# Kernel tuning notes

Hardware: AMD Instinct MI355X
Metric: run time of the kernel (lower is better)

Reference implementation:

```python
import jax, jax.numpy as jnp
import numpy as np
import math

L = 4          # n_layers
H = 8          # n_heads
TOP_K = 32
Z99 = 2.326347874040841
SQRT2PI = math.sqrt(2.0 * math.pi)
CONF = 0.99
SCALE_MAX = 1.0  # model not calibrated -> _scale_max = 1.0
EPS = 1e-5


def layer_norm(x, g, b):
    m = jnp.mean(x, axis=-1, keepdims=True)
    v = jnp.var(x, axis=-1, keepdims=True)
    return (x - m) * jax.lax.rsqrt(v + EPS) * g + b


def pos_encoding(T, D):
    pos = jnp.arange(T, dtype=jnp.float32)[:, None]
    div = jnp.exp(jnp.arange(0, D, 2, dtype=jnp.float32) * (-math.log(10000.0) / D))
    pe = jnp.zeros((T, D), jnp.float32)
    pe = pe.at[:, 0::2].set(jnp.sin(pos * div))
    pe = pe.at[:, 1::2].set(jnp.cos(pos * div))
    return pe  # [T, D]


def sparse_attn(h, Wq, Wk, Wv, Wo, bo):
    B, T, D = h.shape
    dh = D // H
    q = (h @ Wq).reshape(B, T, H, dh)
    k = (h @ Wk).reshape(B, T, H, dh)
    v = (h @ Wv).reshape(B, T, H, dh)
    scores = jnp.einsum('bthd,bshd->bhts', q, k) / np.float32(np.sqrt(dh))  # [B,H,T,T]
    kth = jax.lax.top_k(scores, TOP_K)[0][..., -1:]  # k-th largest per row
    scores = jnp.where(scores < kth, -jnp.inf, scores)
    attn = jax.nn.softmax(scores, axis=-1)
    attn = jnp.nan_to_num(attn)
    out = jnp.einsum('bhts,bshd->bthd', attn, v).reshape(B, T, D)
    return out @ Wo + bo


def encoder_layer(h, Wq, Wk, Wv, Wo, bo, W1, b1, W2, b2, g1, be1, g2, be2):
    h = layer_norm(h + sparse_attn(h, Wq, Wk, Wv, Wo, bo), g1, be1)
    ff = jax.nn.gelu((h @ W1) + b1, approximate=False) @ W2 + b2
    return layer_norm(h + ff, g2, be2)


def setup_inputs() -> dict:
    key = jax.random.key(0)
    B, T, Din, D, Dff = 16, 1024, 64, 512, 2048
    ks = jax.random.split(key, 12)

    def p(k, shape):
        return jax.random.normal(k, shape, jnp.float32) * np.float32(1.0 / np.sqrt(shape[-2]))

    return {
        'x': jax.random.normal(ks[0], (B, T, Din), jnp.float32),
        'W_in': p(ks[1], (Din, D)), 'b_in': jnp.zeros((D,), jnp.float32),
        'Wq': p(ks[2], (L, D, D)), 'Wk': p(ks[3], (L, D, D)),
        'Wv': p(ks[4], (L, D, D)), 'Wo': p(ks[5], (L, D, D)),
        'bo': jnp.zeros((L, D), jnp.float32),
        'W1': p(ks[6], (L, D, Dff)), 'b1': jnp.zeros((L, Dff), jnp.float32),
        'W2': p(ks[7], (L, Dff, D)), 'b2': jnp.zeros((L, D), jnp.float32),
        'g1': jnp.ones((L, D), jnp.float32), 'be1': jnp.zeros((L, D), jnp.float32),
        'g2': jnp.ones((L, D), jnp.float32), 'be2': jnp.zeros((L, D), jnp.float32),
        'gm': jnp.ones((D,), jnp.float32), 'bm': jnp.zeros((D,), jnp.float32),
        'Wm': p(ks[8], (D, 1)), 'cm': jnp.zeros((1,), jnp.float32),
        'gs': jnp.ones((D,), jnp.float32), 'bs': jnp.zeros((D,), jnp.float32),
        'Ws': p(ks[9], (D, 1)), 'cs': jnp.zeros((1,), jnp.float32),
    }


def reference(x, W_in, b_in, Wq, Wk, Wv, Wo, bo, W1, b1, W2, b2, g1, be1, g2, be2,
              gm, bm, Wm, cm, gs, bs, Ws, cs):
    B, T, _ = x.shape
    D = W_in.shape[1]
    h = (x @ W_in) + b_in + pos_encoding(T, D)[None]  # input_proj + pos enc (dropout=eval)
    for i in range(L):
        h = encoder_layer(h, Wq[i], Wk[i], Wv[i], Wo[i], bo[i],
                          W1[i], b1[i], W2[i], b2[i], g1[i], be1[i], g2[i], be2[i])
    h_last = h[:, -1, :]  # [B, D]
    mu = (layer_norm(h_last, gm, bm) @ Wm + cm)[:, 0]
    scale = jax.nn.sigmoid(layer_norm(h_last, gs, bs) @ Ws + cs)[:, 0] * SCALE_MAX
    var_pred = mu + scale * Z99
    phi_z = math.exp(-0.5 * Z99 ** 2) / SQRT2PI
    es_pred = mu + scale * phi_z / (1.0 - CONF)
    return jnp.stack([mu, scale, var_pred, es_pred])  # [4, B]
```

## Files before the change

### kernel.cpp

```cpp
#include <hip/hip_runtime.h>
#include <math.h>


typedef unsigned int u32;
typedef __attribute__((ext_vector_type(8))) _Float16 f16x8;
typedef __attribute__((ext_vector_type(4))) float f32x4;

__device__ __forceinline__ void g2l16(const void* g, void* l) {
  __builtin_amdgcn_global_load_lds(
      (const __attribute__((address_space(1))) u32*)g,
      (__attribute__((address_space(3))) u32*)l, 16, 0, 0);
}

__device__ __forceinline__ void wsplit(float w, unsigned short* ph, unsigned short* pl) {
  _Float16 hi = (_Float16)w;
  _Float16 lo = (_Float16)(w - (float)hi);
  union { _Float16 h; unsigned short u; } a, b; a.h = hi; b.h = lo;
  *ph = a.u; *pl = b.u;
}

__global__ __launch_bounds__(256) void wprep_kernel(const float* __restrict__ src,
    unsigned short* __restrict__ dst_hi, unsigned short* __restrict__ dst_lo,
    int K, int N) {
  __shared__ float t[64][65];
  const int k0 = blockIdx.y * 64, n0 = blockIdx.x * 64;
#pragma unroll
  for (int i = 0; i < 16; i++) {
    int idx = threadIdx.x + i * 256;
    int kk = idx >> 6, nn = idx & 63;
    t[kk][nn] = src[(size_t)(k0 + kk) * N + n0 + nn];
  }
  __syncthreads();
#pragma unroll
  for (int i = 0; i < 16; i++) {
    int idx = threadIdx.x + i * 256;
    int nn = idx >> 6, kk = idx & 63;
    unsigned short uh, ul;
    wsplit(t[kk][nn], &uh, &ul);
    dst_hi[(size_t)(n0 + nn) * K + k0 + kk] = uh;
    dst_lo[(size_t)(n0 + nn) * K + k0 + kk] = ul;
  }
}

__global__ __launch_bounds__(256) void wprep4_kernel(
    const float* __restrict__ s0, const float* __restrict__ s1,
    const float* __restrict__ s2, const float* __restrict__ s3,
    unsigned short* __restrict__ h0, unsigned short* __restrict__ h1,
    unsigned short* __restrict__ h2, unsigned short* __restrict__ h3,
    unsigned short* __restrict__ l0, unsigned short* __restrict__ l1,
    unsigned short* __restrict__ l2, unsigned short* __restrict__ l3) {
  __shared__ float t[64][65];
  const float* src = blockIdx.z == 0 ? s0 : blockIdx.z == 1 ? s1 : blockIdx.z == 2 ? s2 : s3;
  unsigned short* dh = blockIdx.z == 0 ? h0 : blockIdx.z == 1 ? h1 : blockIdx.z == 2 ? h2 : h3;
  unsigned short* dl = blockIdx.z == 0 ? l0 : blockIdx.z == 1 ? l1 : blockIdx.z == 2 ? l2 : l3;
  const int k0 = blockIdx.y * 64, n0 = blockIdx.x * 64;
#pragma unroll
  for (int i = 0; i < 16; i++) {
    int idx = threadIdx.x + i * 256;
    int kk = idx >> 6, nn = idx & 63;
    t[kk][nn] = src[(size_t)(k0 + kk) * 512 + n0 + nn];
  }
  __syncthreads();
#pragma unroll
  for (int i = 0; i < 16; i++) {
    int idx = threadIdx.x + i * 256;
    int nn = idx >> 6, kk = idx & 63;
    unsigned short uh, ul;
    wsplit(t[kk][nn], &uh, &ul);
    dh[(size_t)(n0 + nn) * 512 + k0 + kk] = uh;
    dl[(size_t)(n0 + nn) * 512 + k0 + kk] = ul;
  }
}

__global__ __launch_bounds__(256) void gemm_split(const float* __restrict__ A,
    const unsigned short* __restrict__ Bhi, const unsigned short* __restrict__ Blo,
    const float* __restrict__ bias, float* __restrict__ C,
    unsigned short* __restrict__ Ph, unsigned short* __restrict__ Pl,
    int M, int N, int K, int ldb, int epi) {
  __shared__ float          As[128 * 64];
  __shared__ unsigned short BsH[128 * 64];
  __shared__ unsigned short BsL[128 * 64];
  const int tid = threadIdx.x;
  const int w = tid >> 6, l = tid & 63;
  const int wm = w >> 1, wn = w & 1;
  const int bm = blockIdx.y * 128, bn = blockIdx.x * 128;
  f32x4 acc[4][4] = {};

  for (int k0 = 0; k0 < K; k0 += 64) {
    if (k0) __syncthreads();
#pragma unroll
    for (int i = 0; i < 8; i++) {
      int cl = i * 256 + w * 64 + l;
      int row = cl >> 4, c = cl & 15;
      int col = (((c >> 1) ^ (row & 7)) * 8) + (c & 1) * 4;
      g2l16(A + (size_t)(bm + row) * K + k0 + col, As + (size_t)(i * 256 + w * 64) * 4);
    }
#pragma unroll
    for (int i = 0; i < 4; i++) {
      int cl = i * 256 + w * 64 + l;
      int row = cl >> 3, c = cl & 7;
      int col = ((c ^ (row & 7)) * 8);
      size_t src = (size_t)(bn + row) * ldb + k0 + col;
      g2l16(Bhi + src, BsH + (size_t)(i * 256 + w * 64) * 8);
      g2l16(Blo + src, BsL + (size_t)(i * 256 + w * 64) * 8);
    }
    __syncthreads();
#pragma unroll
    for (int kk = 0; kk < 2; kk++) {
      f16x8 ahi[4], alo[4], bhi[4], blo[4];
      const int c16 = kk * 4 + (l >> 4);
#pragma unroll
      for (int i = 0; i < 4; i++) {
        int ar = wm * 64 + i * 16 + (l & 15);
        const float* ap = &As[ar * 64 + ((c16 ^ (ar & 7)) * 8)];
        float4 a0 = *(const float4*)ap;
        float4 a1 = *(const float4*)(ap + 4);
        float av[8] = {a0.x, a0.y, a0.z, a0.w, a1.x, a1.y, a1.z, a1.w};
#pragma unroll
        for (int e = 0; e < 8; e++) {
          _Float16 hh = (_Float16)av[e];
          ahi[i][e] = hh;
          alo[i][e] = (_Float16)(av[e] - (float)hh);
        }
        int br = wn * 64 + i * 16 + (l & 15);
        bhi[i] = *(const f16x8*)&BsH[br * 64 + ((c16 ^ (br & 7)) * 8)];
        blo[i] = *(const f16x8*)&BsL[br * 64 + ((c16 ^ (br & 7)) * 8)];
      }
#pragma unroll
      for (int i = 0; i < 4; i++)
#pragma unroll
        for (int j = 0; j < 4; j++) {
          acc[i][j] = __builtin_amdgcn_mfma_f32_16x16x32_f16(ahi[i], bhi[j], acc[i][j], 0, 0, 0);
          acc[i][j] = __builtin_amdgcn_mfma_f32_16x16x32_f16(alo[i], bhi[j], acc[i][j], 0, 0, 0);
          acc[i][j] = __builtin_amdgcn_mfma_f32_16x16x32_f16(ahi[i], blo[j], acc[i][j], 0, 0, 0);
        }
    }
  }

  if (epi == 5) {
#pragma unroll
    for (int i = 0; i < 4; i++)
#pragma unroll
      for (int e = 0; e < 4; e++) {
        int row = bm + wm * 64 + i * 16 + (l >> 4) * 4 + e;
#pragma unroll
        for (int j = 0; j < 4; j++) {
          int col = bn + wn * 64 + j * 16 + (l & 15);
          float vv = acc[i][j][e];
          unsigned short uh, ul;
          wsplit(vv, &uh, &ul);
          size_t off = (size_t)(row >> 10) * 524288 + (size_t)(col >> 6) * 65536
                     + (size_t)(row & 1023) * 64 + (col & 63);
          Ph[off] = uh; Pl[off] = ul;
        }
      }
    return;
  }

  float bj[4], fr[4];
#pragma unroll
  for (int j = 0; j < 4; j++) {
    int col = bn + wn * 64 + j * 16 + (l & 15);
    bj[j] = (bias != nullptr) ? bias[col] : 0.f;
    fr[j] = (epi == 3) ? __expf((float)(col & ~1) * (-9.210340371976184f / 512.0f)) : 0.f;
  }
#pragma unroll
  for (int i = 0; i < 4; i++) {
#pragma unroll
    for (int e = 0; e < 4; e++) {
      int row = bm + wm * 64 + i * 16 + (l >> 4) * 4 + e;
#pragma unroll
      for (int j = 0; j < 4; j++) {
        int col = bn + wn * 64 + j * 16 + (l & 15);
        float v = acc[i][j][e] + bj[j];
        if (epi == 2) v = 0.5f * v * (1.0f + erff(v * 0.70710678118654752f));
        if (epi == 3) {
          float ang = (float)(row & 1023) * fr[j];
          v += (col & 1) ? cosf(ang) : sinf(ang);
        }
        if (epi == 4) v += C[(size_t)row * N + col];
        C[(size_t)row * N + col] = v;
      }
    }
  }
}

__device__ __forceinline__ unsigned f2o(float f) {
  unsigned b = __float_as_uint(f);
  return (b & 0x80000000u) ? ~b : (b | 0x80000000u);
}
__device__ __forceinline__ float o2f(unsigned u) {
  unsigned b = (u & 0x80000000u) ? (u & 0x7fffffffu) : ~u;
  return __uint_as_float(b);
}

__global__ __launch_bounds__(512, 4) void attn_kernel(
    const unsigned short* __restrict__ qh, const unsigned short* __restrict__ ql,
    const unsigned short* __restrict__ kh, const unsigned short* __restrict__ kl,
    const float* __restrict__ va, float* __restrict__ ao) {
  __shared__ __align__(16) float smem[14464];
  unsigned short* Qhs = (unsigned short*)smem;
  unsigned short* Qls = Qhs + 2048;
  unsigned short* Khs = Qhs + 4096;
  unsigned short* Kls = Qhs + 12288;
  float* S    = smem + 10240;
  float* cval = smem + 2048;
  int*   cidx = (int*)smem + 5376;

  const int tid = threadIdx.x;
  const int wave = tid >> 6, lane = tid & 63;
  const int id = blockIdx.x;
  const int bh = (id >> 8) * 8 + (id & 7);
  const int t0 = ((id >> 3) & 31) * 32;
  const int b = bh >> 3, hh = bh & 7;
  const size_t hoff = (size_t)bh * 65536;
  const float* vb = va + (size_t)b * 524288 + hh * 64;

  {
    int plane = tid >> 8, cl = tid & 255;
    int row = cl >> 3, c = cl & 7;
    size_t src = hoff + (size_t)(t0 + row) * 64 + ((c ^ (row & 7)) * 8);
    g2l16((plane ? ql : qh) + src, (plane ? Qls : Qhs) + cl * 8);
  }

  float sc[4][16];

  for (int kt = 0; kt < 8; ++kt) {
#pragma unroll
    for (int i = 0; i < 2; ++i) {
      int cl = tid + i * 512;
      int row = cl >> 3, c = cl & 7;
      size_t src = hoff + (size_t)(kt * 128 + row) * 64 + ((c ^ (row & 7)) * 8);
      g2l16(kh + src, Khs + cl * 8);
      g2l16(kl + src, Kls + cl * 8);
    }
    __syncthreads();

    f32x4 a0 = {}, a1 = {};
#pragma unroll
    for (int ks = 0; ks < 2; ++ks) {
      int c = (lane >> 4) + ks * 4;
      int kr = wave * 16 + (lane & 15);
      int ko = kr * 64 + ((c ^ (kr & 7)) * 8);
      f16x8 kfh = *(const f16x8*)&Khs[ko];
      f16x8 kfl = *(const f16x8*)&Kls[ko];
      int q0 = lane & 15;
      int o0 = q0 * 64 + ((c ^ (q0 & 7)) * 8);
      f16x8 qf0h = *(const f16x8*)&Qhs[o0];
      f16x8 qf0l = *(const f16x8*)&Qls[o0];
      int q1 = 16 + (lane & 15);
      int o1 = q1 * 64 + ((c ^ (q1 & 7)) * 8);
      f16x8 qf1h = *(const f16x8*)&Qhs[o1];
      f16x8 qf1l = *(const f16x8*)&Qls[o1];
      a0 = __builtin_amdgcn_mfma_f32_16x16x32_f16(kfh, qf0h, a0, 0, 0, 0);
      a0 = __builtin_amdgcn_mfma_f32_16x16x32_f16(kfl, qf0h, a0, 0, 0, 0);
      a0 = __builtin_amdgcn_mfma_f32_16x16x32_f16(kfh, qf0l, a0, 0, 0, 0);
      a1 = __builtin_amdgcn_mfma_f32_16x16x32_f16(kfh, qf1h, a1, 0, 0, 0);
      a1 = __builtin_amdgcn_mfma_f32_16x16x32_f16(kfl, qf1h, a1, 0, 0, 0);
      a1 = __builtin_amdgcn_mfma_f32_16x16x32_f16(kfh, qf1l, a1, 0, 0, 0);
    }
#pragma unroll
    for (int e = 0; e < 4; ++e) {
      int srow = wave * 16 + (lane >> 4) * 4 + e;
      S[srow * 33 + (lane & 15)]      = a0[e];
      S[srow * 33 + 16 + (lane & 15)] = a1[e];
    }
    __syncthreads();
#pragma unroll
    for (int r = 0; r < 4; ++r) {
      int qr = wave * 4 + r;
      sc[r][kt * 2]     = S[lane * 33 + qr] * 0.125f;
      sc[r][kt * 2 + 1] = S[(64 + lane) * 33 + qr] * 0.125f;
    }
    __syncthreads();
  }

  unsigned uu[4][16];
#pragma unroll
  for (int r = 0; r < 4; ++r)
#pragma unroll
    for (int j = 0; j < 16; ++j) uu[r][j] = f2o(sc[r][j]);

#pragma unroll
  for (int r = 0; r < 4; ++r) {
    const int row = wave * 4 + r;
    unsigned m = uu[r][0];
#pragma unroll
    for (int j = 1; j < 16; ++j) m = m > uu[r][j] ? m : uu[r][j];
    unsigned gm = m;
#pragma unroll
    for (int off = 32; off; off >>= 1) {
      unsigned o = __shfl_xor(gm, off);
      gm = gm > o ? gm : o;
    }
    unsigned lam = 0;
    for (int bit = 31; bit >= 16; --bit) {
      unsigned tv = lam | (1u << bit);
      if (__popcll(__ballot(m >= tv)) >= 32) lam = tv;
    }
    int base = 0;
#pragma unroll
    for (int j = 0; j < 16; ++j) {
      bool p = uu[r][j] >= lam;
      unsigned long long mk = __ballot(p);
      int pos = base + (int)__popcll(mk & ((1ull << lane) - 1ull));
      if (p && pos < 96) { cval[row * 104 + pos] = o2f(uu[r][j]); cidx[row * 104 + pos] = j * 64 + lane; }
      base += (int)__popcll(mk);
    }
    int C = base;
    unsigned kth = 0;
    if (C <= 96) {
      unsigned cu0 = (lane < C)      ? f2o(cval[row * 104 + lane])      : 0u;
      unsigned cu1 = (64 + lane < C) ? f2o(cval[row * 104 + 64 + lane]) : 0u;
      for (int bit = 31; bit >= 0; --bit) {
        unsigned tv = kth | (1u << bit);
        int c = (int)__popcll(__ballot(cu0 >= tv)) + (int)__popcll(__ballot(cu1 >= tv));
        if (c >= 32) kth = tv;
      }
    } else {
      for (int bit = 31; bit >= 0; --bit) {
        unsigned tv = kth | (1u << bit);
        int pc = 0;
#pragma unroll
        for (int j = 0; j < 16; ++j) pc += (uu[r][j] >= tv) ? 1 : 0;
#pragma unroll
        for (int off = 32; off; off >>= 1) pc += __shfl_xor(pc, off);
        if (pc >= 32) kth = tv;
      }
      base = 0;
#pragma unroll
      for (int j = 0; j < 16; ++j) {
        bool p = uu[r][j] >= kth;
        unsigned long long mk = __ballot(p);
        int pos = base + (int)__popcll(mk & ((1ull << lane) - 1ull));
        if (p && pos < 96) { cval[row * 104 + pos] = o2f(uu[r][j]); cidx[row * 104 + pos] = j * 64 + lane; }
        base += (int)__popcll(mk);
      }
      C = base < 96 ? base : 96;
    }
    float kth_f = o2f(kth), gm_f = o2f(gm);
    float e0 = 0.f, e1 = 0.f;
    if (lane < C)      { float vv = cval[row * 104 + lane];      if (vv >= kth_f) e0 = __expf(vv - gm_f); }
    if (64 + lane < C) { float vv = cval[row * 104 + 64 + lane]; if (vv >= kth_f) e1 = __expf(vv - gm_f); }
    float ps = e0 + e1;
#pragma unroll
    for (int off = 32; off; off >>= 1) ps += __shfl_xor(ps, off);
    cval[row * 104 + lane] = e0;
    if (lane < 32) cval[row * 104 + 64 + lane] = e1;
    if (lane < 8)  cval[row * 104 + 96 + lane] = 0.f;
    { int p = C + lane;      if (p < 104) cidx[row * 104 + p] = 0; }
    { int p = C + 64 + lane; if (p < 104) cidx[row * 104 + p] = 0; }

    float acc = 0.f;
    int C8 = (C + 7) & ~7;
    for (int i0 = 0; i0 < C8; i0 += 8) {
      float4 ev0 = *(const float4*)&cval[row * 104 + i0];
      float4 ev1 = *(const float4*)&cval[row * 104 + i0 + 4];
      int4  si0 = *(const int4*)&cidx[row * 104 + i0];
      int4  si1 = *(const int4*)&cidx[row * 104 + i0 + 4];
      float v0 = vb[(size_t)(si0.x & 1023) * 512 + lane];
      float v1 = vb[(size_t)(si0.y & 1023) * 512 + lane];
      float v2 = vb[(size_t)(si0.z & 1023) * 512 + lane];
      float v3 = vb[(size_t)(si0.w & 1023) * 512 + lane];
      float v4 = vb[(size_t)(si1.x & 1023) * 512 + lane];
      float v5 = vb[(size_t)(si1.y & 1023) * 512 + lane];
      float v6 = vb[(size_t)(si1.z & 1023) * 512 + lane];
      float v7 = vb[(size_t)(si1.w & 1023) * 512 + lane];
      acc = fmaf(ev0.x, v0, acc); acc = fmaf(ev0.y, v1, acc);
      acc = fmaf(ev0.z, v2, acc); acc = fmaf(ev0.w, v3, acc);
      acc = fmaf(ev1.x, v4, acc); acc = fmaf(ev1.y, v5, acc);
      acc = fmaf(ev1.z, v6, acc); acc = fmaf(ev1.w, v7, acc);
    }
    ao[((size_t)(b * 1024 + t0 + row)) * 512 + hh * 64 + lane] = acc * (1.f / ps);
  }
}

__global__ __launch_bounds__(256) void resid_ln_kernel(float* __restrict__ h,
    const float* __restrict__ o, const float* __restrict__ g,
    const float* __restrict__ be) {
  const int wave = threadIdx.x >> 6, lane = threadIdx.x & 63;
  const size_t row = (size_t)blockIdx.x * 4 + wave;
  float* hr = h + row * 512;
  const float* orr = o + row * 512;
  float x[8]; float s = 0.f, s2 = 0.f;
#pragma unroll
  for (int j = 0; j < 8; j++) {
    float vv = hr[j * 64 + lane] + orr[j * 64 + lane];
    x[j] = vv; s += vv; s2 += vv * vv;
  }
#pragma unroll
  for (int off = 32; off; off >>= 1) { s += __shfl_xor(s, off); s2 += __shfl_xor(s2, off); }
  float mean = s * (1.f / 512.f);
  float var  = s2 * (1.f / 512.f) - mean * mean;
  float r = rsqrtf(var + 1e-5f);
#pragma unroll
  for (int j = 0; j < 8; j++) {
    int d = j * 64 + lane;
    hr[d] = (x[j] - mean) * r * g[d] + be[d];
  }
}

__global__ __launch_bounds__(256) void head_kernel(const float* __restrict__ h,
    const float* __restrict__ gm, const float* __restrict__ bm,
    const float* __restrict__ Wm, const float* __restrict__ cm,
    const float* __restrict__ gs, const float* __restrict__ bs,
    const float* __restrict__ Ws, const float* __restrict__ cs,
    float* __restrict__ out) {
  const int wave = threadIdx.x >> 6, lane = threadIdx.x & 63;
  const int b = blockIdx.x * 4 + wave;
  const float* hr = h + ((size_t)b * 1024 + 1023) * 512;
  float x[8]; float s = 0.f, s2 = 0.f;
#pragma unroll
  for (int j = 0; j < 8; j++) { float vv = hr[j * 64 + lane]; x[j] = vv; s += vv; s2 += vv * vv; }
#pragma unroll
  for (int off = 32; off; off >>= 1) { s += __shfl_xor(s, off); s2 += __shfl_xor(s2, off); }
  float mean = s * (1.f / 512.f);
  float var  = s2 * (1.f / 512.f) - mean * mean;
  float r = rsqrtf(var + 1e-5f);
  float am = 0.f, as = 0.f;
#pragma unroll
  for (int j = 0; j < 8; j++) {
    int d = j * 64 + lane;
    float n = (x[j] - mean) * r;
    am = fmaf(n * gm[d] + bm[d], Wm[d], am);
    as = fmaf(n * gs[d] + bs[d], Ws[d], as);
  }
#pragma unroll
  for (int off = 32; off; off >>= 1) { am += __shfl_xor(am, off); as += __shfl_xor(as, off); }
  if (lane == 0) {
    const double Z = 2.326347874040841;
    float mu  = am + cm[0];
    float scl = 1.f / (1.f + expf(-(as + cs[0])));
    float esc = (float)(exp(-0.5 * Z * Z) / sqrt(2.0 * 3.14159265358979323846) / 0.01);
    out[b]      = mu;
    out[16 + b] = scl;
    out[32 + b] = mu + scl * (float)Z;
    out[48 + b] = mu + scl * esc;
  }
}

extern "C" void kernel_launch(void* const* d_in, const int* in_sizes, int n_in,
                              void* d_out, int out_size, void* d_ws, size_t ws_size,
                              hipStream_t stream) {
  const float* x    = (const float*)d_in[0];
  const float* W_in = (const float*)d_in[1];
  const float* b_in = (const float*)d_in[2];
  const float* Wq   = (const float*)d_in[3];
  const float* Wk   = (const float*)d_in[4];
  const float* Wv   = (const float*)d_in[5];
  const float* Wo   = (const float*)d_in[6];
  const float* bo   = (const float*)d_in[7];
  const float* W1   = (const float*)d_in[8];
  const float* b1   = (const float*)d_in[9];
  const float* W2   = (const float*)d_in[10];
  const float* b2   = (const float*)d_in[11];
  const float* g1   = (const float*)d_in[12];
  const float* be1  = (const float*)d_in[13];
  const float* g2   = (const float*)d_in[14];
  const float* be2  = (const float*)d_in[15];
  const float* gm   = (const float*)d_in[16];
  const float* bm   = (const float*)d_in[17];
  const float* Wm   = (const float*)d_in[18];
  const float* cm   = (const float*)d_in[19];
  const float* gs   = (const float*)d_in[20];
  const float* bs   = (const float*)d_in[21];
  const float* Ws   = (const float*)d_in[22];
  const float* cs   = (const float*)d_in[23];

  const int M = 16384, D = 512, DFF = 2048;
  float* ws = (float*)d_ws;
  float* h   = ws;
  unsigned short* qhp = (unsigned short*)(ws + 8388608);
  unsigned short* qlp = qhp + 8388608;
  unsigned short* khp = (unsigned short*)(ws + 16777216);
  unsigned short* klp = khp + 8388608;
  float* v   = ws + 25165824;
  float* ao  = ws + 33554432;
  float* ff  = ws + 8388608;
  unsigned short* wl = (unsigned short*)(ws + 41943040);
  unsigned short* WqH = wl,            *WqL = wl + 262144;
  unsigned short* WkH = wl + 524288,   *WkL = wl + 786432;
  unsigned short* WvH = wl + 1048576,  *WvL = wl + 1310720;
  unsigned short* WoH = wl + 1572864,  *WoL = wl + 1835008;
  unsigned short* W1H = wl + 2097152,  *W1L = wl + 3145728;
  unsigned short* W2H = wl + 4194304,  *W2L = wl + 5242880;
  unsigned short* WinH = (unsigned short*)(ws + 45088768);
  unsigned short* WinL = WinH + 32768;

  dim3 blk(256);
  dim3 gD(4, 128);
  dim3 gH(8, 128);

  wprep_kernel<<<dim3(8, 1, 1), blk, 0, stream>>>(W_in, WinH, WinL, 64, 512);
  gemm_split<<<gD, blk, 0, stream>>>(x, WinH, WinL, b_in, h, nullptr, nullptr, M, D, 64, 64, 3);

  for (int l = 0; l < 4; l++) {
    const float* wq = Wq + (size_t)l * 262144;
    const float* wk = Wk + (size_t)l * 262144;
    const float* wv = Wv + (size_t)l * 262144;
    const float* wo = Wo + (size_t)l * 262144;
    const float* w1 = W1 + (size_t)l * 1048576;
    const float* w2 = W2 + (size_t)l * 1048576;

    wprep4_kernel<<<dim3(8, 8, 4), blk, 0, stream>>>(wq, wk, wv, wo,
        WqH, WkH, WvH, WoH, WqL, WkL, WvL, WoL);
    wprep_kernel<<<dim3(32, 8, 1), blk, 0, stream>>>(w1, W1H, W1L, 512, 2048);
    wprep_kernel<<<dim3(8, 32, 1), blk, 0, stream>>>(w2, W2H, W2L, 2048, 512);

    gemm_split<<<gD, blk, 0, stream>>>(h, WqH, WqL, nullptr, nullptr, qhp, qlp, M, D, D, D, 5);
    gemm_split<<<gD, blk, 0, stream>>>(h, WkH, WkL, nullptr, nullptr, khp, klp, M, D, D, D, 5);
    gemm_split<<<gD, blk, 0, stream>>>(h, WvH, WvL, nullptr, v, nullptr, nullptr, M, D, D, D, 1);

    attn_kernel<<<dim3(4096), dim3(512), 0, stream>>>(qhp, qlp, khp, klp, v, ao);

    gemm_split<<<gD, blk, 0, stream>>>(ao, WoH, WoL, bo + (size_t)l * D, v, nullptr, nullptr, M, D, D, D, 1);
    resid_ln_kernel<<<dim3(4096), blk, 0, stream>>>(h, v, g1 + (size_t)l * D, be1 + (size_t)l * D);

    gemm_split<<<gH, blk, 0, stream>>>(h, W1H, W1L, b1 + (size_t)l * DFF, ff, nullptr, nullptr, M, 1024, D, D, 2);
    gemm_split<<<gD, blk, 0, stream>>>(ff, W2H, W2L, nullptr, ao, nullptr, nullptr, M, D, 1024, DFF, 1);
    gemm_split<<<gH, blk, 0, stream>>>(h, W1H + 524288, W1L + 524288,
                                       b1 + (size_t)l * DFF + 1024, ff, nullptr, nullptr, M, 1024, D, D, 2);
    gemm_split<<<gD, blk, 0, stream>>>(ff, W2H + 1024, W2L + 1024,
                                       b2 + (size_t)l * D, ao, nullptr, nullptr, M, D, 1024, DFF, 4);

    resid_ln_kernel<<<dim3(4096), blk, 0, stream>>>(h, ao, g2 + (size_t)l * D, be2 + (size_t)l * D);
  }

  head_kernel<<<dim3(4), blk, 0, stream>>>(h, gm, bm, Wm, cm, gs, bs, Ws, cs, (float*)d_out);
}
```

Baseline: 3.107 ms.

## Store GEMM A-operands as pre-split fp16 hi/lo pairs across all producers

```diff
diff --git a/kernel.cpp b/kernel.cpp
--- a/kernel.cpp
+++ b/kernel.cpp
@@ -17,6 +17,10 @@
   _Float16 lo = (_Float16)(w - (float)hi);
   union { _Float16 h; unsigned short u; } a, b; a.h = hi; b.h = lo;
   *ph = a.u; *pl = b.u;
+}
+
+__device__ __forceinline__ float h2f(unsigned short u) {
+  union { _Float16 h; unsigned short u; } x; x.u = u; return (float)x.h;
 }
 
 __global__ __launch_bounds__(256) void wprep_kernel(const float* __restrict__ src,
@@ -72,12 +76,24 @@
   }
 }
 
-__global__ __launch_bounds__(256) void gemm_split(const float* __restrict__ A,
+__global__ __launch_bounds__(256) void xsplit_kernel(const float* __restrict__ in,
+    unsigned short* __restrict__ oh, unsigned short* __restrict__ ol, int n) {
+  int i = (blockIdx.x * 256 + threadIdx.x) * 4;
+  if (i < n) {
+    float4 v = *(const float4*)(in + i);
+    wsplit(v.x, oh + i, ol + i);     wsplit(v.y, oh + i + 1, ol + i + 1);
+    wsplit(v.z, oh + i + 2, ol + i + 2); wsplit(v.w, oh + i + 3, ol + i + 3);
+  }
+}
+
+__global__ __launch_bounds__(256) void gemm_split(
+    const unsigned short* __restrict__ Ahi, const unsigned short* __restrict__ Alo,
     const unsigned short* __restrict__ Bhi, const unsigned short* __restrict__ Blo,
     const float* __restrict__ bias, float* __restrict__ C,
     unsigned short* __restrict__ Ph, unsigned short* __restrict__ Pl,
     int M, int N, int K, int ldb, int epi) {
-  __shared__ float          As[128 * 64];
+  __shared__ unsigned short AsH[128 * 64];
+  __shared__ unsigned short AsL[128 * 64];
   __shared__ unsigned short BsH[128 * 64];
   __shared__ unsigned short BsL[128 * 64];
   const int tid = threadIdx.x;
@@ -89,20 +105,17 @@
   for (int k0 = 0; k0 < K; k0 += 64) {
     if (k0) __syncthreads();
 #pragma unroll
-    for (int i = 0; i < 8; i++) {
-      int cl = i * 256 + w * 64 + l;
-      int row = cl >> 4, c = cl & 15;
-      int col = (((c >> 1) ^ (row & 7)) * 8) + (c & 1) * 4;
-      g2l16(A + (size_t)(bm + row) * K + k0 + col, As + (size_t)(i * 256 + w * 64) * 4);
-    }
-#pragma unroll
     for (int i = 0; i < 4; i++) {
       int cl = i * 256 + w * 64 + l;
       int row = cl >> 3, c = cl & 7;
       int col = ((c ^ (row & 7)) * 8);
-      size_t src = (size_t)(bn + row) * ldb + k0 + col;
-      g2l16(Bhi + src, BsH + (size_t)(i * 256 + w * 64) * 8);
-      g2l16(Blo + src, BsL + (size_t)(i * 256 + w * 64) * 8);
+      size_t asrc = (size_t)(bm + row) * K + k0 + col;
+      size_t bsrc = (size_t)(bn + row) * ldb + k0 + col;
+      size_t dst = (size_t)(i * 256 + w * 64) * 8;
+      g2l16(Ahi + asrc, AsH + dst);
+      g2l16(Alo + asrc, AsL + dst);
+      g2l16(Bhi + bsrc, BsH + dst);
+      g2l16(Blo + bsrc, BsL + dst);
     }
     __syncthreads();
 #pragma unroll
@@ -112,19 +125,13 @@
 #pragma unroll
       for (int i = 0; i < 4; i++) {
         int ar = wm * 64 + i * 16 + (l & 15);
-        const float* ap = &As[ar * 64 + ((c16 ^ (ar & 7)) * 8)];
-        float4 a0 = *(const float4*)ap;
-        float4 a1 = *(const float4*)(ap + 4);
-        float av[8] = {a0.x, a0.y, a0.z, a0.w, a1.x, a1.y, a1.z, a1.w};
-#pragma unroll
-        for (int e = 0; e < 8; e++) {
-          _Float16 hh = (_Float16)av[e];
-          ahi[i][e] = hh;
-          alo[i][e] = (_Float16)(av[e] - (float)hh);
-        }
+        int aof = ar * 64 + ((c16 ^ (ar & 7)) * 8);
+        ahi[i] = *(const f16x8*)&AsH[aof];
+        alo[i] = *(const f16x8*)&AsL[aof];
         int br = wn * 64 + i * 16 + (l & 15);
-        bhi[i] = *(const f16x8*)&BsH[br * 64 + ((c16 ^ (br & 7)) * 8)];
-        blo[i] = *(const f16x8*)&BsL[br * 64 + ((c16 ^ (br & 7)) * 8)];
+        int bof = br * 64 + ((c16 ^ (br & 7)) * 8);
+        bhi[i] = *(const f16x8*)&BsH[bof];
+        blo[i] = *(const f16x8*)&BsL[bof];
       }
 #pragma unroll
       for (int i = 0; i < 4; i++)
@@ -137,26 +144,6 @@
     }
   }
 
-  if (epi == 5) {
-#pragma unroll
-    for (int i = 0; i < 4; i++)
-#pragma unroll
-      for (int e = 0; e < 4; e++) {
-        int row = bm + wm * 64 + i * 16 + (l >> 4) * 4 + e;
-#pragma unroll
-        for (int j = 0; j < 4; j++) {
-          int col = bn + wn * 64 + j * 16 + (l & 15);
-          float vv = acc[i][j][e];
-          unsigned short uh, ul;
-          wsplit(vv, &uh, &ul);
-          size_t off = (size_t)(row >> 10) * 524288 + (size_t)(col >> 6) * 65536
-                     + (size_t)(row & 1023) * 64 + (col & 63);
-          Ph[off] = uh; Pl[off] = ul;
-        }
-      }
-    return;
-  }
-
   float bj[4], fr[4];
 #pragma unroll
   for (int j = 0; j < 4; j++) {
@@ -173,13 +160,21 @@
       for (int j = 0; j < 4; j++) {
         int col = bn + wn * 64 + j * 16 + (l & 15);
         float v = acc[i][j][e] + bj[j];
-        if (epi == 2) v = 0.5f * v * (1.0f + erff(v * 0.70710678118654752f));
-        if (epi == 3) {
+        if (epi == 2) {
+          v = 0.5f * v * (1.0f + erff(v * 0.70710678118654752f));
+          wsplit(v, Ph + (size_t)row * N + col, Pl + (size_t)row * N + col);
+        } else if (epi == 3) {
           float ang = (float)(row & 1023) * fr[j];
           v += (col & 1) ? cosf(ang) : sinf(ang);
+          wsplit(v, Ph + (size_t)row * N + col, Pl + (size_t)row * N + col);
+        } else if (epi == 5) {
+          size_t off = (size_t)(row >> 10) * 524288 + (size_t)(col >> 6) * 65536
+                     + (size_t)(row & 1023) * 64 + (col & 63);
+          wsplit(v, Ph + off, Pl + off);
+        } else {
+          if (epi == 4) v += C[(size_t)row * N + col];
+          C[(size_t)row * N + col] = v;
         }
-        if (epi == 4) v += C[(size_t)row * N + col];
-        C[(size_t)row * N + col] = v;
       }
     }
   }
@@ -197,7 +192,8 @@
 __global__ __launch_bounds__(512, 4) void attn_kernel(
     const unsigned short* __restrict__ qh, const unsigned short* __restrict__ ql,
     const unsigned short* __restrict__ kh, const unsigned short* __restrict__ kl,
-    const float* __restrict__ va, float* __restrict__ ao) {
+    const float* __restrict__ va,
+    unsigned short* __restrict__ aoh, unsigned short* __restrict__ aol) {
   __shared__ __align__(16) float smem[14464];
   unsigned short* Qhs = (unsigned short*)smem;
   unsigned short* Qls = Qhs + 2048;
@@ -371,21 +367,23 @@
       acc = fmaf(ev1.x, v4, acc); acc = fmaf(ev1.y, v5, acc);
       acc = fmaf(ev1.z, v6, acc); acc = fmaf(ev1.w, v7, acc);
     }
-    ao[((size_t)(b * 1024 + t0 + row)) * 512 + hh * 64 + lane] = acc * (1.f / ps);
-  }
-}
-
-__global__ __launch_bounds__(256) void resid_ln_kernel(float* __restrict__ h,
+    size_t off = ((size_t)(b * 1024 + t0 + row)) * 512 + hh * 64 + lane;
+    wsplit(acc * (1.f / ps), aoh + off, aol + off);
+  }
+}
+
+__global__ __launch_bounds__(256) void resid_ln_kernel(
+    unsigned short* __restrict__ hh, unsigned short* __restrict__ hl,
     const float* __restrict__ o, const float* __restrict__ g,
     const float* __restrict__ be) {
   const int wave = threadIdx.x >> 6, lane = threadIdx.x & 63;
   const size_t row = (size_t)blockIdx.x * 4 + wave;
-  float* hr = h + row * 512;
-  const float* orr = o + row * 512;
+  const size_t rb = row * 512;
   float x[8]; float s = 0.f, s2 = 0.f;
 #pragma unroll
   for (int j = 0; j < 8; j++) {
-    float vv = hr[j * 64 + lane] + orr[j * 64 + lane];
+    size_t idx = rb + j * 64 + lane;
+    float vv = h2f(hh[idx]) + h2f(hl[idx]) + o[idx];
     x[j] = vv; s += vv; s2 += vv * vv;
   }
 #pragma unroll
@@ -396,11 +394,13 @@
 #pragma unroll
   for (int j = 0; j < 8; j++) {
     int d = j * 64 + lane;
-    hr[d] = (x[j] - mean) * r * g[d] + be[d];
-  }
-}
-
-__global__ __launch_bounds__(256) void head_kernel(const float* __restrict__ h,
+    float vv = (x[j] - mean) * r * g[d] + be[d];
+    wsplit(vv, hh + rb + d, hl + rb + d);
+  }
+}
+
+__global__ __launch_bounds__(256) void head_kernel(
+    const unsigned short* __restrict__ hh, const unsigned short* __restrict__ hl,
     const float* __restrict__ gm, const float* __restrict__ bm,
     const float* __restrict__ Wm, const float* __restrict__ cm,
     const float* __restrict__ gs, const float* __restrict__ bs,
@@ -408,10 +408,14 @@
     float* __restrict__ out) {
   const int wave = threadIdx.x >> 6, lane = threadIdx.x & 63;
   const int b = blockIdx.x * 4 + wave;
-  const float* hr = h + ((size_t)b * 1024 + 1023) * 512;
+  const size_t rb = ((size_t)b * 1024 + 1023) * 512;
   float x[8]; float s = 0.f, s2 = 0.f;
 #pragma unroll
-  for (int j = 0; j < 8; j++) { float vv = hr[j * 64 + lane]; x[j] = vv; s += vv; s2 += vv * vv; }
+  for (int j = 0; j < 8; j++) {
+    size_t idx = rb + j * 64 + lane;
+    float vv = h2f(hh[idx]) + h2f(hl[idx]);
+    x[j] = vv; s += vv; s2 += vv * vv;
+  }
 #pragma unroll
   for (int off = 32; off; off >>= 1) { s += __shfl_xor(s, off); s2 += __shfl_xor(s2, off); }
   float mean = s * (1.f / 512.f);
@@ -469,14 +473,17 @@
 
   const int M = 16384, D = 512, DFF = 2048;
   float* ws = (float*)d_ws;
-  float* h   = ws;
+  unsigned short* hh  = (unsigned short*)ws;
+  unsigned short* hl  = hh + 8388608;
   unsigned short* qhp = (unsigned short*)(ws + 8388608);
   unsigned short* qlp = qhp + 8388608;
   unsigned short* khp = (unsigned short*)(ws + 16777216);
   unsigned short* klp = khp + 8388608;
   float* v   = ws + 25165824;
-  float* ao  = ws + 33554432;
-  float* ff  = ws + 8388608;
+  unsigned short* aoh = (unsigned short*)(ws + 33554432);
+  unsigned short* aol = aoh + 8388608;
+  unsigned short* ffh = (unsigned short*)(ws + 8388608);
+  unsigned short* ffl = (unsigned short*)(ws + 16777216);
   unsigned short* wl = (unsigned short*)(ws + 41943040);
   unsigned short* WqH = wl,            *WqL = wl + 262144;
   unsigned short* WkH = wl + 524288,   *WkL = wl + 786432;
@@ -486,13 +493,16 @@
   unsigned short* W2H = wl + 4194304,  *W2L = wl + 5242880;
   unsigned short* WinH = (unsigned short*)(ws + 45088768);
   unsigned short* WinL = WinH + 32768;
+  unsigned short* xh   = (unsigned short*)(ws + 45121536);
+  unsigned short* xl   = xh + 1048576;
 
   dim3 blk(256);
   dim3 gD(4, 128);
   dim3 gH(8, 128);
 
   wprep_kernel<<<dim3(8, 1, 1), blk, 0, stream>>>(W_in, WinH, WinL, 64, 512);
-  gemm_split<<<gD, blk, 0, stream>>>(x, WinH, WinL, b_in, h, nullptr, nullptr, M, D, 64, 64, 3);
+  xsplit_kernel<<<dim3(1024), blk, 0, stream>>>(x, xh, xl, M * 64);
+  gemm_split<<<gD, blk, 0, stream>>>(xh, xl, WinH, WinL, b_in, nullptr, hh, hl, M, D, 64, 64, 3);
 
   for (int l = 0; l < 4; l++) {
     const float* wq = Wq + (size_t)l * 262144;
@@ -507,24 +517,24 @@
     wprep_kernel<<<dim3(32, 8, 1), blk, 0, stream>>>(w1, W1H, W1L, 512, 2048);
     wprep_kernel<<<dim3(8, 32, 1), blk, 0, stream>>>(w2, W2H, W2L, 2048, 512);
 
-    gemm_split<<<gD, blk, 0, stream>>>(h, WqH, WqL, nullptr, nullptr, qhp, qlp, M, D, D, D, 5);
-    gemm_split<<<gD, blk, 0, stream>>>(h, WkH, WkL, nullptr, nullptr, khp, klp, M, D, D, D, 5);
-    gemm_split<<<gD, blk, 0, stream>>>(h, WvH, WvL, nullptr, v, nullptr, nullptr, M, D, D, D, 1);
-
-    attn_kernel<<<dim3(4096), dim3(512), 0, stream>>>(qhp, qlp, khp, klp, v, ao);
-
-    gemm_split<<<gD, blk, 0, stream>>>(ao, WoH, WoL, bo + (size_t)l * D, v, nullptr, nullptr, M, D, D, D, 1);
-    resid_ln_kernel<<<dim3(4096), blk, 0, stream>>>(h, v, g1 + (size_t)l * D, be1 + (size_t)l * D);
-
-    gemm_split<<<gH, blk, 0, stream>>>(h, W1H, W1L, b1 + (size_t)l * DFF, ff, nullptr, nullptr, M, 1024, D, D, 2);
-    gemm_split<<<gD, blk, 0, stream>>>(ff, W2H, W2L, nullptr, ao, nullptr, nullptr, M, D, 1024, DFF, 1);
-    gemm_split<<<gH, blk, 0, stream>>>(h, W1H + 524288, W1L + 524288,
-                                       b1 + (size_t)l * DFF + 1024, ff, nullptr, nullptr, M, 1024, D, D, 2);
-    gemm_split<<<gD, blk, 0, stream>>>(ff, W2H + 1024, W2L + 1024,
-                                       b2 + (size_t)l * D, ao, nullptr, nullptr, M, D, 1024, DFF, 4);
-
-    resid_ln_kernel<<<dim3(4096), blk, 0, stream>>>(h, ao, g2 + (size_t)l * D, be2 + (size_t)l * D);
-  }
-
-  head_kernel<<<dim3(4), blk, 0, stream>>>(h, gm, bm, Wm, cm, gs, bs, Ws, cs, (float*)d_out);
-}
+    gemm_split<<<gD, blk, 0, stream>>>(hh, hl, WqH, WqL, nullptr, nullptr, qhp, qlp, M, D, D, D, 5);
+    gemm_split<<<gD, blk, 0, stream>>>(hh, hl, WkH, WkL, nullptr, nullptr, khp, klp, M, D, D, D, 5);
+    gemm_split<<<gD, blk, 0, stream>>>(hh, hl, WvH, WvL, nullptr, v, nullptr, nullptr, M, D, D, D, 1);
+
+    attn_kernel<<<dim3(4096), dim3(512), 0, stream>>>(qhp, qlp, khp, klp, v, aoh, aol);
+
+    gemm_split<<<gD, blk, 0, stream>>>(aoh, aol, WoH, WoL, bo + (size_t)l * D, v, nullptr, nullptr, M, D, D, D, 1);
+    resid_ln_kernel<<<dim3(4096), blk, 0, stream>>>(hh, hl, v, g1 + (size_t)l * D, be1 + (size_t)l * D);
+
+    gemm_split<<<gH, blk, 0, stream>>>(hh, hl, W1H, W1L, b1 + (size_t)l * DFF, nullptr, ffh, ffl, M, 1024, D, D, 2);
+    gemm_split<<<gD, blk, 0, stream>>>(ffh, ffl, W2H, W2L, nullptr, v, nullptr, nullptr, M, D, 1024, DFF, 1);
+    gemm_split<<<gH, blk, 0, stream>>>(hh, hl, W1H + 524288, W1L + 524288,
+                                       b1 + (size_t)l * DFF + 1024, nullptr, ffh, ffl, M, 1024, D, D, 2);
+    gemm_split<<<gD, blk, 0, stream>>>(ffh, ffl, W2H + 1024, W2L + 1024,
+                                       b2 + (size_t)l * D, v, nullptr, nullptr, M, D, 1024, DFF, 4);
+
+    resid_ln_kernel<<<dim3(4096), blk, 0, stream>>>(hh, hl, v, g2 + (size_t)l * D, be2 + (size_t)l * D);
+  }
+
+  head_kernel<<<dim3(4), blk, 0, stream>>>(hh, hl, gm, bm, Wm, cm, gs, bs, Ws, cs, (float*)d_out);
+}
```

Result: slower. 7.646 ms (+146.1%).
